# Optimization experiments

Hardware: AMD Instinct MI355X
Metric: run time of the kernel (lower is better)

Reference implementation:

```python
import jax, jax.numpy as jnp
import numpy as np

N_NODES = 100000
N_EDGES = 3200000
IN_CH = 32
EDGE_DIM = 8
HEADS = 8
HIDDEN = 64


def _lin(key, fan_in, fan_out, bias=True):
    k1, k2 = jax.random.split(key)
    s = 1.0 / np.sqrt(fan_in)
    w = jax.random.uniform(k1, (fan_in, fan_out), jnp.float32, -s, s)
    if bias:
        b = jax.random.uniform(k2, (fan_out,), jnp.float32, -s, s)
        return w, b
    return w


def setup_inputs() -> dict:
    key = jax.random.key(0)
    ks = jax.random.split(key, 40)
    inp = {}
    inp['x'] = jax.random.normal(ks[0], (N_NODES, IN_CH), jnp.float32)
    inp['edge_index'] = jax.random.randint(ks[1], (2, N_EDGES), 0, N_NODES, jnp.int32)
    inp['edge_attr'] = jax.random.normal(ks[2], (N_EDGES, EDGE_DIM), jnp.float32)
    # layer dims: (in, heads, out_per_head)
    dims = [(IN_CH, HEADS, 6), (HEADS * 6, HEADS, 3), (HEADS * 3, 1, HIDDEN)]
    ki = 3
    for li, (cin, H, C) in enumerate(dims, start=1):
        HC = H * C
        inp[f'wq{li}'], inp[f'bq{li}'] = _lin(ks[ki], cin, HC); ki += 1
        inp[f'wk{li}'], inp[f'bk{li}'] = _lin(ks[ki], cin, HC); ki += 1
        inp[f'wv{li}'], inp[f'bv{li}'] = _lin(ks[ki], cin, HC); ki += 1
        inp[f'we{li}'] = _lin(ks[ki], EDGE_DIM, HC, bias=False); ki += 1
        inp[f'wskip{li}'], inp[f'bskip{li}'] = _lin(ks[ki], cin, HC); ki += 1
        inp[f'wbeta{li}'] = _lin(ks[ki], 3 * HC, 1, bias=False); ki += 1
    inp['wc'], inp['bc'] = _lin(ks[ki], HIDDEN, 1)
    return inp


def _transformer_conv(x, src, dst, edge_attr, wq, bq, wk, bk, wv, bv, we, wskip, bskip, wbeta, H, C):
    """PyG TransformerConv (concat=True, beta=True, root_weight=True), eval mode."""
    N = x.shape[0]
    e = (edge_attr @ we).reshape(-1, H, C)                  # [E,H,C]
    q = (x @ wq + bq).reshape(N, H, C)[dst]                 # [E,H,C]
    k = (x @ wk + bk).reshape(N, H, C)[src] + e
    v = (x @ wv + bv).reshape(N, H, C)[src] + e
    logits = (q * k).sum(-1) * (1.0 / np.sqrt(C))           # [E,H]
    # segment softmax over incoming edges of each dst node
    m = jax.ops.segment_max(logits, dst, num_segments=N)
    ex = jnp.exp(logits - m[dst])
    den = jax.ops.segment_sum(ex, dst, num_segments=N)
    alpha = ex / (den[dst] + 1e-16)                         # [E,H]
    out = jax.ops.segment_sum(alpha[:, :, None] * v, dst, num_segments=N)
    out = out.reshape(N, H * C)
    x_r = x @ wskip + bskip
    g = jax.nn.sigmoid(jnp.concatenate([out, x_r, out - x_r], axis=-1) @ wbeta)  # [N,1]
    return g * x_r + (1.0 - g) * out


def reference(x, edge_index, edge_attr,
              wq1, bq1, wk1, bk1, wv1, bv1, we1, wskip1, bskip1, wbeta1,
              wq2, bq2, wk2, bk2, wv2, bv2, we2, wskip2, bskip2, wbeta2,
              wq3, bq3, wk3, bk3, wv3, bv3, we3, wskip3, bskip3, wbeta3,
              wc, bc):
    src, dst = edge_index[0], edge_index[1]
    h = _transformer_conv(x, src, dst, edge_attr, wq1, bq1, wk1, bk1, wv1, bv1, we1, wskip1, bskip1, wbeta1, HEADS, 6)
    h = jax.nn.relu(h)
    h = _transformer_conv(h, src, dst, edge_attr, wq2, bq2, wk2, bk2, wv2, bv2, we2, wskip2, bskip2, wbeta2, HEADS, 3)
    h = jax.nn.relu(h)
    h = _transformer_conv(h, src, dst, edge_attr, wq3, bq3, wk3, bk3, wv3, bv3, we3, wskip3, bskip3, wbeta3, 1, HIDDEN)
    h = jax.nn.relu(h)
    logits = (h @ wc + bc).squeeze(-1)                      # [N]
    return logits
```

## Files before the change

### kernel.cpp

```cpp
#include <hip/hip_runtime.h>
#include <hip/hip_fp16.h>
#include <math.h>

#define RCHUNK 8192
#define NBUCK 512
#define CAP 12288

__device__ __forceinline__ float2 H2F(unsigned u) {
    __half2 h = *reinterpret_cast<__half2*>(&u);
    return __half22float2(h);
}
__device__ __forceinline__ unsigned F2H(float a, float b) {
    __half2 h = __floats2half2_rn(a, b);
    return *reinterpret_cast<unsigned*>(&h);
}

__device__ __forceinline__ void loadA(const __half* p, float* a) {
    uint4 u = *(const uint4*)p;
    float2 t;
    t = H2F(u.x); a[0] = t.x; a[1] = t.y;
    t = H2F(u.y); a[2] = t.x; a[3] = t.y;
    t = H2F(u.z); a[4] = t.x; a[5] = t.y;
    t = H2F(u.w); a[6] = t.x; a[7] = t.y;
}

template<int C>
__device__ __forceinline__ void loadKV(const __half* p, float* k, float* v) {
    if constexpr (C == 6) {
        uint4 p0 = *(const uint4*)p;
        uint4 p1 = *(const uint4*)(p + 8);
        float2 t;
        t = H2F(p0.x); k[0] = t.x; k[1] = t.y;
        t = H2F(p0.y); k[2] = t.x; k[3] = t.y;
        t = H2F(p0.z); k[4] = t.x; k[5] = t.y;
        t = H2F(p0.w); v[0] = t.x; v[1] = t.y;
        t = H2F(p1.x); v[2] = t.x; v[3] = t.y;
        t = H2F(p1.y); v[4] = t.x; v[5] = t.y;
    } else {
        uint4 p0 = *(const uint4*)p;
        float2 t;
        t = H2F(p0.x); k[0] = t.x; k[1] = t.y;
        t = H2F(p0.y); k[2] = t.x; v[0] = t.y;
        t = H2F(p0.z); v[1] = t.x; v[2] = t.y;
    }
}

__global__ void histA_kernel(const int* __restrict__ ei, int* __restrict__ hist,
                             int E, int nblk) {
    __shared__ int h[NBUCK];
    h[threadIdx.x] = 0;
    h[threadIdx.x + 256] = 0;
    __syncthreads();
    int base = blockIdx.x * RCHUNK;
#pragma unroll
    for (int r = 0; r < RCHUNK / 256; ++r) {
        int i = base + r * 256 + threadIdx.x;
        if (i < E) atomicAdd(&h[ei[E + i] >> 8], 1);
    }
    __syncthreads();
    hist[threadIdx.x * nblk + blockIdx.x] = h[threadIdx.x];
    hist[(threadIdx.x + 256) * nblk + blockIdx.x] = h[threadIdx.x + 256];
}

__global__ void scanB_kernel(int* __restrict__ hist, int* __restrict__ btot, int nblk) {
    __shared__ int sm[1024];
    int b = blockIdx.x;
    int tid = threadIdx.x;
    int v = (tid < nblk) ? hist[b * nblk + tid] : 0;
    sm[tid] = v;
    __syncthreads();
    for (int off = 1; off < 1024; off <<= 1) {
        int t = (tid >= off) ? sm[tid - off] : 0;
        __syncthreads();
        sm[tid] += t;
        __syncthreads();
    }
    if (tid < nblk) hist[b * nblk + tid] = sm[tid] - v;
    if (tid == 1023) btot[b] = sm[1023];
}

__global__ void scanC_kernel(const int* __restrict__ btot, int* __restrict__ bbase) {
    __shared__ int sm[NBUCK];
    int tid = threadIdx.x;
    int v = btot[tid];
    sm[tid] = v;
    __syncthreads();
    for (int off = 1; off < NBUCK; off <<= 1) {
        int t = (tid >= off) ? sm[tid - off] : 0;
        __syncthreads();
        sm[tid] += t;
        __syncthreads();
    }
    bbase[tid] = sm[tid] - v;
}

__global__ void reorderB_kernel(const int* __restrict__ ei, const int* __restrict__ hist,
                                const int* __restrict__ bbase, unsigned* __restrict__ sorted,
                                int E, int nblk) {
    __shared__ int off[NBUCK];
    off[threadIdx.x] = bbase[threadIdx.x] + hist[threadIdx.x * nblk + blockIdx.x];
    off[threadIdx.x + 256] = bbase[threadIdx.x + 256] + hist[(threadIdx.x + 256) * nblk + blockIdx.x];
    __syncthreads();
    int base = blockIdx.x * RCHUNK;
#pragma unroll
    for (int r = 0; r < RCHUNK / 256; ++r) {
        int i = base + r * 256 + threadIdx.x;
        if (i < E) {
            int dst = ei[E + i];
            int k = atomicAdd(&off[dst >> 8], 1);
            sorted[k] = ((unsigned)(dst & 255) << 24) | (unsigned)i;
        }
    }
}

__global__ __launch_bounds__(256) void bucketsort_kernel(
        const unsigned* __restrict__ sorted,
        const int* __restrict__ bbase, const int* __restrict__ btot,
        int* __restrict__ rowptr,
        const int* __restrict__ ei, const float* __restrict__ ea,
        int* __restrict__ srcp, __half* __restrict__ eap, int N, int E) {
    __shared__ int h[256];
    __shared__ int tmp[CAP];
    int b = blockIdx.x;
    int lo = b << 8;
    int s = bbase[b], cnt = btot[b];
    int tid = threadIdx.x;

    h[tid] = 0;
    __syncthreads();
    for (int i = tid; i < cnt; i += 256) atomicAdd(&h[sorted[s + i] >> 24], 1);
    __syncthreads();
    int v = h[tid];
    for (int off = 1; off < 256; off <<= 1) {
        int t = (tid >= off) ? h[tid - off] : 0;
        __syncthreads();
        h[tid] += t;
        __syncthreads();
    }
    int excl = h[tid] - v;
    int dst = lo + tid;
    if (dst < N) rowptr[dst] = s + excl;
    if (b == 0 && tid == 0) rowptr[N] = E;
    __syncthreads();
    h[tid] = excl;
    __syncthreads();
    for (int i = tid; i < cnt; i += 256) {
        unsigned p2 = sorted[s + i];
        int dl = p2 >> 24;
        int eid = p2 & 0xFFFFFF;
        int r = atomicAdd(&h[dl], 1);
        if (r < CAP) {
            tmp[r] = eid;
        } else {
            int slot = s + r;
            srcp[slot] = ei[eid];
            float4 a0 = *(const float4*)(ea + (size_t)eid * 8);
            float4 a1 = *(const float4*)(ea + (size_t)eid * 8 + 4);
            uint4 u;
            u.x = F2H(a0.x, a0.y); u.y = F2H(a0.z, a0.w);
            u.z = F2H(a1.x, a1.y); u.w = F2H(a1.z, a1.w);
            *(uint4*)(eap + (size_t)slot * 8) = u;
        }
    }
    __syncthreads();
    int m = cnt < CAP ? cnt : CAP;
    for (int j = tid; j < m; j += 256) {
        int eid = tmp[j];
        int slot = s + j;
        srcp[slot] = ei[eid];
        float4 a0 = *(const float4*)(ea + (size_t)eid * 8);
        float4 a1 = *(const float4*)(ea + (size_t)eid * 8 + 4);
        uint4 u;
        u.x = F2H(a0.x, a0.y); u.y = F2H(a0.z, a0.w);
        u.z = F2H(a1.x, a1.y); u.w = F2H(a1.z, a1.w);
        *(uint4*)(eap + (size_t)slot * 8) = u;
    }
}

template<int CIN, int C, int PK>
__global__ void proj8_kernel(const float* __restrict__ X,
                             const float* __restrict__ wq, const float* __restrict__ bq,
                             const float* __restrict__ wk, const float* __restrict__ bk,
                             const float* __restrict__ wv, const float* __restrict__ bv,
                             const float* __restrict__ wsk, const float* __restrict__ bsk,
                             float* __restrict__ Q, __half* __restrict__ KV,
                             float* __restrict__ S, int N)
{
    const int HC = 8 * C;
    int idx = blockIdx.x * blockDim.x + threadIdx.x;
    if (idx >= N * HC) return;
    int n = idx / HC;
    int c = idx - n * HC;
    int h = c / C;
    int cc = c - h * C;
    float q = bq[c], k = bk[c], v = bv[c], s = bsk[c];
    const float* xr = X + (size_t)n * CIN;
#pragma unroll
    for (int i = 0; i < CIN; ++i) {
        float xi = xr[i];
        q = fmaf(xi, wq[i * HC + c], q);
        k = fmaf(xi, wk[i * HC + c], k);
        v = fmaf(xi, wv[i * HC + c], v);
        s = fmaf(xi, wsk[i * HC + c], s);
    }
    Q[(size_t)n * HC + c] = q;
    __half* kp = KV + (size_t)n * (8 * PK) + h * PK;
    kp[cc] = __float2half_rn(k);
    kp[C + cc] = __float2half_rn(v);
    S[(size_t)n * HC + c] = s;
}

__global__ void proj64_kernel(const float* __restrict__ X,
                              const float* __restrict__ wq, const float* __restrict__ bq,
                              const float* __restrict__ wk, const float* __restrict__ bk,
                              const float* __restrict__ wv, const float* __restrict__ bv,
                              const float* __restrict__ wsk, const float* __restrict__ bsk,
                              float* __restrict__ Q, __half* __restrict__ K16,
                              __half* __restrict__ V16, float* __restrict__ S, int N)
{
    int idx = blockIdx.x * blockDim.x + threadIdx.x;
    if (idx >= N * 64) return;
    int n = idx >> 6;
    int c = idx & 63;
    float q = bq[c], k = bk[c], v = bv[c], s = bsk[c];
    const float* xr = X + (size_t)n * 24;
#pragma unroll
    for (int i = 0; i < 24; ++i) {
        float xi = xr[i];
        q = fmaf(xi, wq[i * 64 + c], q);
        k = fmaf(xi, wk[i * 64 + c], k);
        v = fmaf(xi, wv[i * 64 + c], v);
        s = fmaf(xi, wsk[i * 64 + c], s);
    }
    Q[idx] = q;
    K16[idx] = __float2half_rn(k);
    V16[idx] = __float2half_rn(v);
    S[idx] = s;
}

template<int C, int PK, int UNR>
__global__ void gather8f_kernel(const int* __restrict__ rowptr,
                                const int* __restrict__ srcp,
                                const __half* __restrict__ eap,
                                const float* __restrict__ we,
                                const float* __restrict__ Q,
                                const __half* __restrict__ KV,
                                const float* __restrict__ S,
                                const float* __restrict__ wb,
                                float* __restrict__ OUT,
                                int N, float scale)
{
    const int HC = 8 * C;
    int tid = blockIdx.x * blockDim.x + threadIdx.x;
    int n = tid >> 3;
    int h = tid & 7;
    if (n >= N) return;

    float q[C];
    const float* Qp = Q + (size_t)n * HC + h * C;
#pragma unroll
    for (int c = 0; c < C; ++c) q[c] = Qp[c];

    float qe[8];
#pragma unroll
    for (int d = 0; d < 8; ++d) {
        float t = 0.f;
#pragma unroll
        for (int c = 0; c < C; ++c) t = fmaf(we[d * HC + h * C + c], q[c], t);
        qe[d] = t;
    }

    float num[C];
#pragma unroll
    for (int c = 0; c < C; ++c) num[c] = 0.f;
    float sacc[8];
#pragma unroll
    for (int d = 0; d < 8; ++d) sacc[d] = 0.f;
    float den = 0.f;

    int rs = rowptr[n], re = rowptr[n + 1];
    int j = rs;
    for (; j + UNR - 1 < re; j += UNR) {
        int se[UNR];
        float a[UNR][8], kk[UNR][C], vv[UNR][C];
#pragma unroll
        for (int u = 0; u < UNR; ++u) se[u] = srcp[j + u];
#pragma unroll
        for (int u = 0; u < UNR; ++u) loadA(eap + (size_t)(j + u) * 8, a[u]);
#pragma unroll
        for (int u = 0; u < UNR; ++u)
            loadKV<C>(KV + (size_t)se[u] * (8 * PK) + h * PK, kk[u], vv[u]);
        float ex[UNR];
#pragma unroll
        for (int u = 0; u < UNR; ++u) {
            float d0 = 0.f;
#pragma unroll
            for (int c = 0; c < C; ++c) d0 = fmaf(q[c], kk[u][c], d0);
            float qa = 0.f;
#pragma unroll
            for (int d = 0; d < 8; ++d) qa = fmaf(qe[d], a[u][d], qa);
            ex[u] = __expf((d0 + qa) * scale);
        }
#pragma unroll
        for (int u = 0; u < UNR; ++u) {
            den += ex[u];
#pragma unroll
            for (int c = 0; c < C; ++c) num[c] = fmaf(ex[u], vv[u][c], num[c]);
#pragma unroll
            for (int d = 0; d < 8; ++d) sacc[d] = fmaf(ex[u], a[u][d], sacc[d]);
        }
    }
    for (; j < re; ++j) {
        int s0 = srcp[j];
        float a0[8];
        loadA(eap + (size_t)j * 8, a0);
        float k0[C], v0[C];
        loadKV<C>(KV + (size_t)s0 * (8 * PK) + h * PK, k0, v0);
        float d0 = 0.f;
#pragma unroll
        for (int c = 0; c < C; ++c) d0 = fmaf(q[c], k0[c], d0);
        float qa0 = 0.f;
#pragma unroll
        for (int d = 0; d < 8; ++d) qa0 = fmaf(qe[d], a0[d], qa0);
        float ex0 = __expf((d0 + qa0) * scale);
        den += ex0;
#pragma unroll
        for (int c = 0; c < C; ++c) num[c] = fmaf(ex0, v0[c], num[c]);
#pragma unroll
        for (int d = 0; d < 8; ++d) sacc[d] = fmaf(ex0, a0[d], sacc[d]);
    }

    float inv = 1.f / (den + 1e-16f);
    float outc[C], sc[C];
    float gd = 0.f;
#pragma unroll
    for (int c = 0; c < C; ++c) {
        float e_ = 0.f;
#pragma unroll
        for (int d = 0; d < 8; ++d) e_ = fmaf(we[d * HC + h * C + c], sacc[d], e_);
        float o = (num[c] + e_) * inv;
        float s_ = S[(size_t)n * HC + h * C + c];
        outc[c] = o;
        sc[c] = s_;
        gd += o * wb[h * C + c] + s_ * wb[HC + h * C + c] + (o - s_) * wb[2 * HC + h * C + c];
    }
    gd += __shfl_xor(gd, 1, 8);
    gd += __shfl_xor(gd, 2, 8);
    gd += __shfl_xor(gd, 4, 8);
    float g = 1.f / (1.f + __expf(-gd));
#pragma unroll
    for (int c = 0; c < C; ++c) {
        float hh = fmaxf(g * sc[c] + (1.f - g) * outc[c], 0.f);
        OUT[(size_t)n * HC + h * C + c] = hh;
    }
}

__global__ void gather64f_kernel(const int* __restrict__ rowptr,
                                 const int* __restrict__ srcp,
                                 const __half* __restrict__ eap,
                                 const float* __restrict__ we,
                                 const float* __restrict__ Q,
                                 const __half* __restrict__ K16,
                                 const __half* __restrict__ V16,
                                 const float* __restrict__ S,
                                 const float* __restrict__ wb,
                                 const float* __restrict__ wc,
                                 const float* __restrict__ bc,
                                 float* __restrict__ OUT,
                                 int N, float scale)
{
    int grp = (blockIdx.x * blockDim.x + threadIdx.x) >> 4;
    int l16 = threadIdx.x & 15;
    if (grp >= N) return;
    int c0 = l16 << 2;

    float4 qv = *(const float4*)(Q + (size_t)grp * 64 + c0);
    float qe[8];
#pragma unroll
    for (int d = 0; d < 8; ++d) {
        float4 w4 = *(const float4*)(we + d * 64 + c0);
        float t = w4.x * qv.x;
        t = fmaf(w4.y, qv.y, t);
        t = fmaf(w4.z, qv.z, t);
        t = fmaf(w4.w, qv.w, t);
        qe[d] = t;
    }

    float num0 = 0.f, num1 = 0.f, num2 = 0.f, num3 = 0.f, den = 0.f;
    float sacc[8];
#pragma unroll
    for (int d = 0; d < 8; ++d) sacc[d] = 0.f;

    int rs = rowptr[grp], re = rowptr[grp + 1];
    int j = rs;
    for (; j + 3 < re; j += 4) {
        int se[4];
        float a[4][8];
        uint2 ku[4], vu[4];
#pragma unroll
        for (int u = 0; u < 4; ++u) se[u] = srcp[j + u];
#pragma unroll
        for (int u = 0; u < 4; ++u) loadA(eap + (size_t)(j + u) * 8, a[u]);
#pragma unroll
        for (int u = 0; u < 4; ++u) {
            ku[u] = *(const uint2*)(K16 + (size_t)se[u] * 64 + c0);
            vu[u] = *(const uint2*)(V16 + (size_t)se[u] * 64 + c0);
        }
        float t[4];
#pragma unroll
        for (int u = 0; u < 4; ++u) {
            float2 ka = H2F(ku[u].x), kb = H2F(ku[u].y);
            float tt = qv.x * ka.x;
            tt = fmaf(qv.y, ka.y, tt); tt = fmaf(qv.z, kb.x, tt); tt = fmaf(qv.w, kb.y, tt);
#pragma unroll
            for (int d = 0; d < 8; ++d) tt = fmaf(qe[d], a[u][d], tt);
            t[u] = tt;
        }
#pragma unroll
        for (int off = 8; off > 0; off >>= 1) {
            t[0] += __shfl_xor(t[0], off, 16);
            t[1] += __shfl_xor(t[1], off, 16);
            t[2] += __shfl_xor(t[2], off, 16);
            t[3] += __shfl_xor(t[3], off, 16);
        }
#pragma unroll
        for (int u = 0; u < 4; ++u) {
            float ex = __expf(t[u] * scale);
            den += ex;
            float2 va = H2F(vu[u].x), vb = H2F(vu[u].y);
            num0 = fmaf(ex, va.x, num0);
            num1 = fmaf(ex, va.y, num1);
            num2 = fmaf(ex, vb.x, num2);
            num3 = fmaf(ex, vb.y, num3);
#pragma unroll
            for (int d = 0; d < 8; ++d) sacc[d] = fmaf(ex, a[u][d], sacc[d]);
        }
    }
    for (; j < re; ++j) {
        int s0 = srcp[j];
        float a0[8];
        loadA(eap + (size_t)j * 8, a0);
        uint2 ku0 = *(const uint2*)(K16 + (size_t)s0 * 64 + c0);
        uint2 vu0 = *(const uint2*)(V16 + (size_t)s0 * 64 + c0);
        float2 ka0 = H2F(ku0.x), kb0 = H2F(ku0.y);
        float2 va0 = H2F(vu0.x), vb0 = H2F(vu0.y);
        float t0 = qv.x * ka0.x;
        t0 = fmaf(qv.y, ka0.y, t0); t0 = fmaf(qv.z, kb0.x, t0); t0 = fmaf(qv.w, kb0.y, t0);
#pragma unroll
        for (int d = 0; d < 8; ++d) t0 = fmaf(qe[d], a0[d], t0);
#pragma unroll
        for (int off = 8; off > 0; off >>= 1) t0 += __shfl_xor(t0, off, 16);
        float ex0 = __expf(t0 * scale);
        den += ex0;
        num0 = fmaf(ex0, va0.x, num0);
        num1 = fmaf(ex0, va0.y, num1);
        num2 = fmaf(ex0, vb0.x, num2);
        num3 = fmaf(ex0, vb0.y, num3);
#pragma unroll
        for (int d = 0; d < 8; ++d) sacc[d] = fmaf(ex0, a0[d], sacc[d]);
    }

#pragma unroll
    for (int d = 0; d < 8; ++d) {
        float4 w4 = *(const float4*)(we + d * 64 + c0);
        num0 = fmaf(w4.x, sacc[d], num0);
        num1 = fmaf(w4.y, sacc[d], num1);
        num2 = fmaf(w4.z, sacc[d], num2);
        num3 = fmaf(w4.w, sacc[d], num3);
    }
    float inv = 1.f / (den + 1e-16f);
    float o0 = num0 * inv, o1 = num1 * inv, o2 = num2 * inv, o3 = num3 * inv;
    float4 sv  = *(const float4*)(S + (size_t)grp * 64 + c0);
    float4 wb0 = *(const float4*)(wb + c0);
    float4 wb1 = *(const float4*)(wb + 64 + c0);
    float4 wb2 = *(const float4*)(wb + 128 + c0);
    float gd = o0 * wb0.x + sv.x * wb1.x + (o0 - sv.x) * wb2.x;
    gd += o1 * wb0.y + sv.y * wb1.y + (o1 - sv.y) * wb2.y;
    gd += o2 * wb0.z + sv.z * wb1.z + (o2 - sv.z) * wb2.z;
    gd += o3 * wb0.w + sv.w * wb1.w + (o3 - sv.w) * wb2.w;
#pragma unroll
    for (int off = 8; off > 0; off >>= 1) gd += __shfl_xor(gd, off, 16);
    float g = 1.f / (1.f + __expf(-gd));
    float h0 = fmaxf(g * sv.x + (1.f - g) * o0, 0.f);
    float h1 = fmaxf(g * sv.y + (1.f - g) * o1, 0.f);
    float h2 = fmaxf(g * sv.z + (1.f - g) * o2, 0.f);
    float h3 = fmaxf(g * sv.w + (1.f - g) * o3, 0.f);
    float4 wcv = *(const float4*)(wc + c0);
    float t = h0 * wcv.x + h1 * wcv.y + h2 * wcv.z + h3 * wcv.w;
#pragma unroll
    for (int off = 8; off > 0; off >>= 1) t += __shfl_xor(t, off, 16);
    if (l16 == 0) OUT[grp] = t + bc[0];
}

extern "C" void kernel_launch(void* const* d_in, const int* in_sizes, int n_in,
                              void* d_out, int out_size, void* d_ws, size_t ws_size,
                              hipStream_t stream) {
    const float* x  = (const float*)d_in[0];
    const int*   ei = (const int*)d_in[1];
    const float* ea = (const float*)d_in[2];
    const int N = in_sizes[0] / 32;
    const int E = in_sizes[1] / 2;

    int p = 3;
    const float *wq1=(const float*)d_in[p+0], *bq1=(const float*)d_in[p+1],
                *wk1=(const float*)d_in[p+2], *bk1=(const float*)d_in[p+3],
                *wv1=(const float*)d_in[p+4], *bv1=(const float*)d_in[p+5],
                *we1=(const float*)d_in[p+6],
                *wsk1=(const float*)d_in[p+7], *bsk1=(const float*)d_in[p+8],
                *wb1=(const float*)d_in[p+9];
    p += 10;
    const float *wq2=(const float*)d_in[p+0], *bq2=(const float*)d_in[p+1],
                *wk2=(const float*)d_in[p+2], *bk2=(const float*)d_in[p+3],
                *wv2=(const float*)d_in[p+4], *bv2=(const float*)d_in[p+5],
                *we2=(const float*)d_in[p+6],
                *wsk2=(const float*)d_in[p+7], *bsk2=(const float*)d_in[p+8],
                *wb2=(const float*)d_in[p+9];
    p += 10;
    const float *wq3=(const float*)d_in[p+0], *bq3=(const float*)d_in[p+1],
                *wk3=(const float*)d_in[p+2], *bk3=(const float*)d_in[p+3],
                *wv3=(const float*)d_in[p+4], *bv3=(const float*)d_in[p+5],
                *we3=(const float*)d_in[p+6],
                *wsk3=(const float*)d_in[p+7], *bsk3=(const float*)d_in[p+8],
                *wb3=(const float*)d_in[p+9];
    p += 10;
    const float *wc = (const float*)d_in[p+0], *bc = (const float*)d_in[p+1];

    float* out = (float*)d_out;

    float* ws = (float*)d_ws;
    float* Hb = ws;
    float* Qb = Hb + (size_t)N * 48;
    float* Sb = Qb + (size_t)N * 64;
    __half* KV16  = (__half*)(Sb + (size_t)N * 64);
    __half* K3    = KV16;
    __half* V3    = KV16 + (size_t)N * 64;
    __half* eap16 = KV16 + (size_t)N * 128;
    int* ip      = (int*)(eap16 + (size_t)E * 8);
    int* rowptr  = ip;
    int* btot    = rowptr + (N + 2);
    int* bbase   = btot + 512;
    int* srcp    = bbase + 512;
    int* hist    = srcp + E;
    unsigned* sorted = (unsigned*)Qb;

    const int BLK = 256;
    const int nblkR = (E + RCHUNK - 1) / RCHUNK;
    const int nbuckUsed = (N + 255) >> 8;

    histA_kernel<<<nblkR, 256, 0, stream>>>(ei, hist, E, nblkR);
    scanB_kernel<<<NBUCK, 1024, 0, stream>>>(hist, btot, nblkR);
    scanC_kernel<<<1, NBUCK, 0, stream>>>(btot, bbase);
    reorderB_kernel<<<nblkR, 256, 0, stream>>>(ei, hist, bbase, sorted, E, nblkR);
    bucketsort_kernel<<<nbuckUsed, 256, 0, stream>>>(
        sorted, bbase, btot, rowptr, ei, ea, srcp, eap16, N, E);

    proj8_kernel<32,6,16><<<(N*48 + BLK-1)/BLK, BLK, 0, stream>>>(
        x, wq1,bq1, wk1,bk1, wv1,bv1, wsk1,bsk1, Qb, KV16, Sb, N);
    gather8f_kernel<6,16,2><<<(N*8 + BLK-1)/BLK, BLK, 0, stream>>>(
        rowptr, srcp, eap16, we1, Qb, KV16, Sb, wb1, Hb, N, 1.0f/sqrtf(6.0f));

    proj8_kernel<48,3,8><<<(N*24 + BLK-1)/BLK, BLK, 0, stream>>>(
        Hb, wq2,bq2, wk2,bk2, wv2,bv2, wsk2,bsk2, Qb, KV16, Sb, N);
    gather8f_kernel<3,8,4><<<(N*8 + BLK-1)/BLK, BLK, 0, stream>>>(
        rowptr, srcp, eap16, we2, Qb, KV16, Sb, wb2, Hb, N, 1.0f/sqrtf(3.0f));

    proj64_kernel<<<(N*64 + BLK-1)/BLK, BLK, 0, stream>>>(
        Hb, wq3,bq3, wk3,bk3, wv3,bv3, wsk3,bsk3, Qb, K3, V3, Sb, N);
    gather64f_kernel<<<((size_t)N*16 + BLK-1)/BLK, BLK, 0, stream>>>(
        rowptr, srcp, eap16, we3, Qb, K3, V3, Sb, wb3, wc, bc, out, N, 1.0f/8.0f);
}
```

Baseline: 809.7 us.

## Use 8 lanes per node in final gather with wider loads, nontemporal edge streams

The layer-3 gather kernel now assigns 8 lanes per destination node, each handling 8 channels, instead of 16 lanes handling 4. This halves the redundant per-lane loads of src indices and edge attributes, widens K/V loads to 16 bytes, and shortens the shuffle reductions. Edge attribute and src index loads in both gather kernels also switch to nontemporal loads to reduce cache pollution. The trade-off is more registers per thread and half as many threads in flight to hide gather latency.

```diff
diff --git a/kernel.cpp b/kernel.cpp
--- a/kernel.cpp
+++ b/kernel.cpp
@@ -6,6 +6,8 @@
 #define NBUCK 512
 #define CAP 12288
 
+typedef unsigned ev4 __attribute__((ext_vector_type(4)));
+
 __device__ __forceinline__ float2 H2F(unsigned u) {
     __half2 h = *reinterpret_cast<__half2*>(&u);
     return __half22float2(h);
@@ -15,8 +17,8 @@
     return *reinterpret_cast<unsigned*>(&h);
 }
 
-__device__ __forceinline__ void loadA(const __half* p, float* a) {
-    uint4 u = *(const uint4*)p;
+__device__ __forceinline__ void loadA_nt(const __half* p, float* a) {
+    ev4 u = __builtin_nontemporal_load((const ev4*)p);
     float2 t;
     t = H2F(u.x); a[0] = t.x; a[1] = t.y;
     t = H2F(u.y); a[2] = t.x; a[3] = t.y;
@@ -284,9 +286,9 @@
         int se[UNR];
         float a[UNR][8], kk[UNR][C], vv[UNR][C];
 #pragma unroll
-        for (int u = 0; u < UNR; ++u) se[u] = srcp[j + u];
-#pragma unroll
-        for (int u = 0; u < UNR; ++u) loadA(eap + (size_t)(j + u) * 8, a[u]);
+        for (int u = 0; u < UNR; ++u) se[u] = __builtin_nontemporal_load(&srcp[j + u]);
+#pragma unroll
+        for (int u = 0; u < UNR; ++u) loadA_nt(eap + (size_t)(j + u) * 8, a[u]);
 #pragma unroll
         for (int u = 0; u < UNR; ++u)
             loadKV<C>(KV + (size_t)se[u] * (8 * PK) + h * PK, kk[u], vv[u]);
@@ -313,7 +315,7 @@
     for (; j < re; ++j) {
         int s0 = srcp[j];
         float a0[8];
-        loadA(eap + (size_t)j * 8, a0);
+        loadA_nt(eap + (size_t)j * 8, a0);
         float k0[C], v0[C];
         loadKV<C>(KV + (size_t)s0 * (8 * PK) + h * PK, k0, v0);
         float d0 = 0.f;
@@ -355,83 +357,99 @@
     }
 }
 
-__global__ void gather64f_kernel(const int* __restrict__ rowptr,
-                                 const int* __restrict__ srcp,
-                                 const __half* __restrict__ eap,
-                                 const float* __restrict__ we,
-                                 const float* __restrict__ Q,
-                                 const __half* __restrict__ K16,
-                                 const __half* __restrict__ V16,
-                                 const float* __restrict__ S,
-                                 const float* __restrict__ wb,
-                                 const float* __restrict__ wc,
-                                 const float* __restrict__ bc,
-                                 float* __restrict__ OUT,
-                                 int N, float scale)
+__global__ __launch_bounds__(256) void gather64f_kernel(
+        const int* __restrict__ rowptr,
+        const int* __restrict__ srcp,
+        const __half* __restrict__ eap,
+        const float* __restrict__ we,
+        const float* __restrict__ Q,
+        const __half* __restrict__ K16,
+        const __half* __restrict__ V16,
+        const float* __restrict__ S,
+        const float* __restrict__ wb,
+        const float* __restrict__ wc,
+        const float* __restrict__ bc,
+        float* __restrict__ OUT,
+        int N, float scale)
 {
-    int grp = (blockIdx.x * blockDim.x + threadIdx.x) >> 4;
-    int l16 = threadIdx.x & 15;
+    int grp = (blockIdx.x * blockDim.x + threadIdx.x) >> 3;
+    int l8 = threadIdx.x & 7;
     if (grp >= N) return;
-    int c0 = l16 << 2;
-
-    float4 qv = *(const float4*)(Q + (size_t)grp * 64 + c0);
+    int c0 = l8 << 3;
+
+    float q[8];
+    *(float4*)q       = *(const float4*)(Q + (size_t)grp * 64 + c0);
+    *(float4*)(q + 4) = *(const float4*)(Q + (size_t)grp * 64 + c0 + 4);
     float qe[8];
 #pragma unroll
     for (int d = 0; d < 8; ++d) {
-        float4 w4 = *(const float4*)(we + d * 64 + c0);
-        float t = w4.x * qv.x;
-        t = fmaf(w4.y, qv.y, t);
-        t = fmaf(w4.z, qv.z, t);
-        t = fmaf(w4.w, qv.w, t);
+        float4 w0 = *(const float4*)(we + d * 64 + c0);
+        float4 w1 = *(const float4*)(we + d * 64 + c0 + 4);
+        float t = w0.x * q[0];
+        t = fmaf(w0.y, q[1], t); t = fmaf(w0.z, q[2], t); t = fmaf(w0.w, q[3], t);
+        t = fmaf(w1.x, q[4], t); t = fmaf(w1.y, q[5], t); t = fmaf(w1.z, q[6], t);
+        t = fmaf(w1.w, q[7], t);
         qe[d] = t;
     }
 
-    float num0 = 0.f, num1 = 0.f, num2 = 0.f, num3 = 0.f, den = 0.f;
+    float num[8];
+#pragma unroll
+    for (int c = 0; c < 8; ++c) num[c] = 0.f;
     float sacc[8];
 #pragma unroll
     for (int d = 0; d < 8; ++d) sacc[d] = 0.f;
+    float den = 0.f;
 
     int rs = rowptr[grp], re = rowptr[grp + 1];
     int j = rs;
     for (; j + 3 < re; j += 4) {
         int se[4];
         float a[4][8];
-        uint2 ku[4], vu[4];
-#pragma unroll
-        for (int u = 0; u < 4; ++u) se[u] = srcp[j + u];
-#pragma unroll
-        for (int u = 0; u < 4; ++u) loadA(eap + (size_t)(j + u) * 8, a[u]);
+        uint4 ku[4], vu[4];
+#pragma unroll
+        for (int u = 0; u < 4; ++u) se[u] = __builtin_nontemporal_load(&srcp[j + u]);
+#pragma unroll
+        for (int u = 0; u < 4; ++u) loadA_nt(eap + (size_t)(j + u) * 8, a[u]);
 #pragma unroll
         for (int u = 0; u < 4; ++u) {
-            ku[u] = *(const uint2*)(K16 + (size_t)se[u] * 64 + c0);
-            vu[u] = *(const uint2*)(V16 + (size_t)se[u] * 64 + c0);
+            ku[u] = *(const uint4*)(K16 + (size_t)se[u] * 64 + c0);
+            vu[u] = *(const uint4*)(V16 + (size_t)se[u] * 64 + c0);
         }
         float t[4];
 #pragma unroll
         for (int u = 0; u < 4; ++u) {
-            float2 ka = H2F(ku[u].x), kb = H2F(ku[u].y);
-            float tt = qv.x * ka.x;
-            tt = fmaf(qv.y, ka.y, tt); tt = fmaf(qv.z, kb.x, tt); tt = fmaf(qv.w, kb.y, tt);
+            float2 k01 = H2F(ku[u].x), k23 = H2F(ku[u].y);
+            float2 k45 = H2F(ku[u].z), k67 = H2F(ku[u].w);
+            float tt = q[0] * k01.x;
+            tt = fmaf(q[1], k01.y, tt); tt = fmaf(q[2], k23.x, tt);
+            tt = fmaf(q[3], k23.y, tt); tt = fmaf(q[4], k45.x, tt);
+            tt = fmaf(q[5], k45.y, tt); tt = fmaf(q[6], k67.x, tt);
+            tt = fmaf(q[7], k67.y, tt);
 #pragma unroll
             for (int d = 0; d < 8; ++d) tt = fmaf(qe[d], a[u][d], tt);
             t[u] = tt;
         }
 #pragma unroll
-        for (int off = 8; off > 0; off >>= 1) {
-            t[0] += __shfl_xor(t[0], off, 16);
-            t[1] += __shfl_xor(t[1], off, 16);
-            t[2] += __shfl_xor(t[2], off, 16);
-            t[3] += __shfl_xor(t[3], off, 16);
+        for (int off = 4; off > 0; off >>= 1) {
+            t[0] += __shfl_xor(t[0], off, 8);
+            t[1] += __shfl_xor(t[1], off, 8);
+            t[2] += __shfl_xor(t[2], off, 8);
+            t[3] += __shfl_xor(t[3], off, 8);
         }
 #pragma unroll
         for (int u = 0; u < 4; ++u) {
             float ex = __expf(t[u] * scale);
             den += ex;
-            float2 va = H2F(vu[u].x), vb = H2F(vu[u].y);
-            num0 = fmaf(ex, va.x, num0);
-            num1 = fmaf(ex, va.y, num1);
-            num2 = fmaf(ex, vb.x, num2);
-            num3 = fmaf(ex, vb.y, num3);
+            float2 v01 = H2F(vu[u].x), v23 = H2F(vu[u].y);
+            float2 v45 = H2F(vu[u].z), v67 = H2F(vu[u].w);
+            num[0] = fmaf(ex, v01.x, num[0]);
+            num[1] = fmaf(ex, v01.y, num[1]);
+            num[2] = fmaf(ex, v23.x, num[2]);
+            num[3] = fmaf(ex, v23.y, num[3]);
+            num[4] = fmaf(ex, v45.x, num[4]);
+            num[5] = fmaf(ex, v45.y, num[5]);
+            num[6] = fmaf(ex, v67.x, num[6]);
+            num[7] = fmaf(ex, v67.y, num[7]);
 #pragma unroll
             for (int d = 0; d < 8; ++d) sacc[d] = fmaf(ex, a[u][d], sacc[d]);
         }
@@ -439,57 +457,71 @@
     for (; j < re; ++j) {
         int s0 = srcp[j];
         float a0[8];
-        loadA(eap + (size_t)j * 8, a0);
-        uint2 ku0 = *(const uint2*)(K16 + (size_t)s0 * 64 + c0);
-        uint2 vu0 = *(const uint2*)(V16 + (size_t)s0 * 64 + c0);
-        float2 ka0 = H2F(ku0.x), kb0 = H2F(ku0.y);
-        float2 va0 = H2F(vu0.x), vb0 = H2F(vu0.y);
-        float t0 = qv.x * ka0.x;
-        t0 = fmaf(qv.y, ka0.y, t0); t0 = fmaf(qv.z, kb0.x, t0); t0 = fmaf(qv.w, kb0.y, t0);
+        loadA_nt(eap + (size_t)j * 8, a0);
+        uint4 ku0 = *(const uint4*)(K16 + (size_t)s0 * 64 + c0);
+        uint4 vu0 = *(const uint4*)(V16 + (size_t)s0 * 64 + c0);
+        float2 k01 = H2F(ku0.x), k23 = H2F(ku0.y);
+        float2 k45 = H2F(ku0.z), k67 = H2F(ku0.w);
+        float t0 = q[0] * k01.x;
+        t0 = fmaf(q[1], k01.y, t0); t0 = fmaf(q[2], k23.x, t0);
+        t0 = fmaf(q[3], k23.y, t0); t0 = fmaf(q[4], k45.x, t0);
+        t0 = fmaf(q[5], k45.y, t0); t0 = fmaf(q[6], k67.x, t0);
+        t0 = fmaf(q[7], k67.y, t0);
 #pragma unroll
         for (int d = 0; d < 8; ++d) t0 = fmaf(qe[d], a0[d], t0);
 #pragma unroll
-        for (int off = 8; off > 0; off >>= 1) t0 += __shfl_xor(t0, off, 16);
+        for (int off = 4; off > 0; off >>= 1) t0 += __shfl_xor(t0, off, 8);
         float ex0 = __expf(t0 * scale);
         den += ex0;
-        num0 = fmaf(ex0, va0.x, num0);
-        num1 = fmaf(ex0, va0.y, num1);
-        num2 = fmaf(ex0, vb0.x, num2);
-        num3 = fmaf(ex0, vb0.y, num3);
+        float2 v01 = H2F(vu0.x), v23 = H2F(vu0.y);
+        float2 v45 = H2F(vu0.z), v67 = H2F(vu0.w);
+        num[0] = fmaf(ex0, v01.x, num[0]);
+        num[1] = fmaf(ex0, v01.y, num[1]);
+        num[2] = fmaf(ex0, v23.x, num[2]);
+        num[3] = fmaf(ex0, v23.y, num[3]);
+        num[4] = fmaf(ex0, v45.x, num[4]);
+        num[5] = fmaf(ex0, v45.y, num[5]);
+        num[6] = fmaf(ex0, v67.x, num[6]);
+        num[7] = fmaf(ex0, v67.y, num[7]);
 #pragma unroll
         for (int d = 0; d < 8; ++d) sacc[d] = fmaf(ex0, a0[d], sacc[d]);
     }
 
 #pragma unroll
     for (int d = 0; d < 8; ++d) {
-        float4 w4 = *(const float4*)(we + d * 64 + c0);
-        num0 = fmaf(w4.x, sacc[d], num0);
-        num1 = fmaf(w4.y, sacc[d], num1);
-        num2 = fmaf(w4.z, sacc[d], num2);
-        num3 = fmaf(w4.w, sacc[d], num3);
+        float4 w0 = *(const float4*)(we + d * 64 + c0);
+        float4 w1 = *(const float4*)(we + d * 64 + c0 + 4);
+        num[0] = fmaf(w0.x, sacc[d], num[0]);
+        num[1] = fmaf(w0.y, sacc[d], num[1]);
+        num[2] = fmaf(w0.z, sacc[d], num[2]);
+        num[3] = fmaf(w0.w, sacc[d], num[3]);
+        num[4] = fmaf(w1.x, sacc[d], num[4]);
+        num[5] = fmaf(w1.y, sacc[d], num[5]);
+        num[6] = fmaf(w1.z, sacc[d], num[6]);
+        num[7] = fmaf(w1.w, sacc[d], num[7]);
     }
     float inv = 1.f / (den + 1e-16f);
-    float o0 = num0 * inv, o1 = num1 * inv, o2 = num2 * inv, o3 = num3 * inv;
-    float4 sv  = *(const float4*)(S + (size_t)grp * 64 + c0);
-    float4 wb0 = *(const float4*)(wb + c0);
-    float4 wb1 = *(const float4*)(wb + 64 + c0);
-    float4 wb2 = *(const float4*)(wb + 128 + c0);
-    float gd = o0 * wb0.x + sv.x * wb1.x + (o0 - sv.x) * wb2.x;
-    gd += o1 * wb0.y + sv.y * wb1.y + (o1 - sv.y) * wb2.y;
-    gd += o2 * wb0.z + sv.z * wb1.z + (o2 - sv.z) * wb2.z;
-    gd += o3 * wb0.w + sv.w * wb1.w + (o3 - sv.w) * wb2.w;
-#pragma unroll
-    for (int off = 8; off > 0; off >>= 1) gd += __shfl_xor(gd, off, 16);
+    float o[8], sv[8];
+    *(float4*)sv       = *(const float4*)(S + (size_t)grp * 64 + c0);
+    *(float4*)(sv + 4) = *(const float4*)(S + (size_t)grp * 64 + c0 + 4);
+    float gd = 0.f;
+#pragma unroll
+    for (int c = 0; c < 8; ++c) {
+        o[c] = num[c] * inv;
+        gd += o[c] * wb[c0 + c] + sv[c] * wb[64 + c0 + c] + (o[c] - sv[c]) * wb[128 + c0 + c];
+    }
+#pragma unroll
+    for (int off = 4; off > 0; off >>= 1) gd += __shfl_xor(gd, off, 8);
     float g = 1.f / (1.f + __expf(-gd));
-    float h0 = fmaxf(g * sv.x + (1.f - g) * o0, 0.f);
-    float h1 = fmaxf(g * sv.y + (1.f - g) * o1, 0.f);
-    float h2 = fmaxf(g * sv.z + (1.f - g) * o2, 0.f);
-    float h3 = fmaxf(g * sv.w + (1.f - g) * o3, 0.f);
-    float4 wcv = *(const float4*)(wc + c0);
-    float t = h0 * wcv.x + h1 * wcv.y + h2 * wcv.z + h3 * wcv.w;
-#pragma unroll
-    for (int off = 8; off > 0; off >>= 1) t += __shfl_xor(t, off, 16);
-    if (l16 == 0) OUT[grp] = t + bc[0];
+    float t = 0.f;
+#pragma unroll
+    for (int c = 0; c < 8; ++c) {
+        float hh = fmaxf(g * sv[c] + (1.f - g) * o[c], 0.f);
+        t = fmaf(hh, wc[c0 + c], t);
+    }
+#pragma unroll
+    for (int off = 4; off > 0; off >>= 1) t += __shfl_xor(t, off, 8);
+    if (l8 == 0) OUT[grp] = t + bc[0];
 }
 
 extern "C" void kernel_launch(void* const* d_in, const int* in_sizes, int n_in,
@@ -566,6 +598,6 @@
 
     proj64_kernel<<<(N*64 + BLK-1)/BLK, BLK, 0, stream>>>(
         Hb, wq3,bq3, wk3,bk3, wv3,bv3, wsk3,bsk3, Qb, K3, V3, Sb, N);
-    gather64f_kernel<<<((size_t)N*16 + BLK-1)/BLK, BLK, 0, stream>>>(
+    gather64f_kernel<<<((size_t)N*8 + BLK-1)/BLK, BLK, 0, stream>>>(
         rowptr, srcp, eap16, we3, Qb, K3, V3, Sb, wb3, wc, bc, out, N, 1.0f/8.0f);
 }
```

After: 880.2 us. 1.09x slower.
